# Optimization experiments

Hardware: AMD Instinct MI355X
Metric: run time of the kernel (lower is better)

Reference implementation:

```python
import jax, jax.numpy as jnp
import numpy as np

N = 1200        # nodes in the (complete) graph
SLOPE = 0.1     # leaky_relu negative slope
# smat: 10-vector -> symmetric 4x4
SMAT_IDX = np.array([0,1,2,3,1,4,5,6,2,5,7,8,3,6,8,9])

def _glorot(k, shape):
    lim = float(np.sqrt(6.0 / (shape[0] + shape[1])))
    return jax.random.uniform(k, shape, jnp.float32, -lim, lim)

def setup_inputs():
    key = jax.random.key(0)
    ks = jax.random.split(key, 24)
    # complete graph connectivity (recover_S reads edge_map[i,j] for all i!=j)
    iu, ju = np.triu_indices(N, k=1)
    E = iu.shape[0]
    eid = np.arange(E, dtype=np.int32)
    edge_map = np.zeros((N, N), dtype=np.int32)
    edge_map[iu, ju] = eid
    edge_map[ju, iu] = eid
    ud_edges = np.stack([iu, ju], axis=1).astype(np.int32)           # [E,2]
    edge_index = np.stack([np.concatenate([iu, ju]),
                           np.concatenate([ju, iu])]).astype(np.int32)  # [2,2E]
    inp = {
        'x': jax.random.normal(ks[0], (N, 16), jnp.float32),
        'edge_index': jnp.asarray(edge_index),
        'edge_map': jnp.asarray(edge_map),
        'ud_edges': jnp.asarray(ud_edges),
    }
    dims = {'g': [(6, 32), (32, 32), (32, 64)],
            'n': [(64, 64), (64, 64), (64, 10)],
            'e': [(64, 64), (64, 64), (64, 16)]}
    k = 1
    for tag, ds in dims.items():
        for i, (a, b) in enumerate(ds):
            inp[f'W{tag}{i+1}'] = _glorot(ks[k], (a, b)); k += 1
            inp[f'b{tag}{i+1}'] = jnp.zeros((b,), jnp.float32)
    return inp

def _leaky(v):
    return jnp.where(v >= 0, v, SLOPE * v)

def _gcn(x, src, dst, W, b):
    deg = jax.ops.segment_sum(jnp.ones(src.shape[0], x.dtype), dst, num_segments=N)
    dinv = jnp.where(deg > 0, jax.lax.rsqrt(deg), 0.0)
    norm = dinv[src] * dinv[dst]
    h = x @ W
    return jax.ops.segment_sum(norm[:, None] * h[src], dst, num_segments=N) + b

def _mlp3(h, W1, b1, W2, b2, W3, b3):
    # dropout is identity (eval mode)
    h = _leaky(h @ W1 + b1)
    h = _leaky(h @ W2 + b2)
    return h @ W3 + b3

def _forward(x, edge_index, edge_map, ud_edges,
             Wg1, bg1, Wg2, bg2, Wg3, bg3,
             Wn1, bn1, Wn2, bn2, Wn3, bn3,
             We1, be1, We2, be2, We3, be3):
    x6 = x[:, 0:6]                       # node_feature_mode == 1
    src, dst = edge_index[0], edge_index[1]
    h = _leaky(_gcn(x6, src, dst, Wg1, bg1))
    h = _leaky(_gcn(h, src, dst, Wg2, bg2))
    h = _gcn(h, src, dst, Wg3, bg3)      # [N,64]
    vd = _mlp3(h, Wn1, bn1, Wn2, bn2, Wn3, bn3)            # [N,10]
    he = h[ud_edges[:, 0]] + h[ud_edges[:, 1]]             # [E,64]
    ed = _mlp3(he, We1, be1, We2, be2, We3, be3)           # [E,16]
    # recover_S: block-structured [4N,4N]
    Vsym = vd[:, jnp.asarray(SMAT_IDX)].reshape(N, 4, 4)   # smat per node
    Eb = ed.reshape(-1, 4, 4)
    B = Eb[edge_map]                                       # [N,N,4,4]
    ii = jnp.arange(N)
    lower = ii[:, None] > ii[None, :]
    B = jnp.where(lower[:, :, None, None], jnp.swapaxes(B, 2, 3), B)
    B = B.at[ii, ii].set(Vsym)
    S = B.transpose(0, 2, 1, 3).reshape(4 * N, 4 * N)
    return h, S

def reference(x, edge_index, edge_map, ud_edges,
              Wg1, bg1, Wg2, bg2, Wg3, bg3,
              Wn1, bn1, Wn2, bn2, Wn3, bn3,
              We1, be1, We2, be2, We3, be3):
    return _forward(x, edge_index, edge_map, ud_edges,
                    Wg1, bg1, Wg2, bg2, Wg3, bg3,
                    Wn1, bn1, Wn2, bn2, Wn3, bn3,
                    We1, be1, We2, be2, We3, be3)
```

## Files before the change

kernel.cpp:

```cpp
#include <hip/hip_runtime.h>

#define NN 1200
#define NE 719400
#define SDIM 4800

typedef __attribute__((ext_vector_type(8))) short bf16x8;
typedef __attribute__((ext_vector_type(4))) float f32x4;

static __device__ __constant__ int SMAT[16] = {0,1,2,3,1,4,5,6,2,5,7,8,3,6,8,9};

__device__ __forceinline__ float lk(float v) { return v >= 0.f ? v : 0.1f * v; }

__device__ __forceinline__ void split8(const float* u, bf16x8& hi, bf16x8& lo) {
#pragma unroll
    for (int e = 0; e < 8; e++) {
        unsigned x = __float_as_uint(u[e]);
        unsigned r = x + 0x7FFFu + ((x >> 16) & 1u);
        hi[e] = (short)(r >> 16);
        float hf = __uint_as_float(r & 0xFFFF0000u);
        float s = u[e] - hf;
        unsigned v = __float_as_uint(s);
        unsigned w = v + 0x7FFFu + ((v >> 16) & 1u);
        lo[e] = (short)(w >> 16);
    }
}

__device__ __forceinline__ uint2 split2(float a0, float a1) {
    unsigned u0 = __float_as_uint(a0), u1 = __float_as_uint(a1);
    unsigned r0 = u0 + 0x7FFFu + ((u0 >> 16) & 1u);
    unsigned r1 = u1 + 0x7FFFu + ((u1 >> 16) & 1u);
    float h0 = __uint_as_float(r0 & 0xFFFF0000u);
    float h1 = __uint_as_float(r1 & 0xFFFF0000u);
    float s0 = a0 - h0, s1 = a1 - h1;
    unsigned v0 = __float_as_uint(s0), v1 = __float_as_uint(s1);
    unsigned t0 = v0 + 0x7FFFu + ((v0 >> 16) & 1u);
    unsigned t1 = v1 + 0x7FFFu + ((v1 >> 16) & 1u);
    unsigned hi = (r0 >> 16) | (r1 & 0xFFFF0000u);
    unsigned lo = (t0 >> 16) | (t1 & 0xFFFF0000u);
    return make_uint2(hi, lo);
}

__global__ void k_init(float* cs) {
    int t = threadIdx.x;
    if (t < 128) cs[t] = 0.f;
}

__global__ void k_prep(const float* __restrict__ We2, const float* __restrict__ We3,
                       unsigned* __restrict__ W2F, unsigned* __restrict__ W3F) {
    int t = blockIdx.x * 256 + threadIdx.x;
    if (t < 512) {
        int lane = t & 63, nf = (t >> 6) & 3, ks = t >> 8;
        int n = (lane & 15) + 16 * nf;
        int kb = ks * 32 + (lane >> 4) * 8;
        unsigned* dst = W2F + t * 8;
#pragma unroll
        for (int p = 0; p < 4; p++) {
            float a0 = We2[(kb + 2 * p) * 64 + n];
            float a1 = We2[(kb + 2 * p + 1) * 64 + n];
            uint2 hl = split2(a0, a1);
            dst[p] = hl.x; dst[4 + p] = hl.y;
        }
    } else if (t < 640) {
        int q = t - 512;
        int lane = q & 63, ks = q >> 6;
        int n = lane & 15;
        int kb = ks * 32 + (lane >> 4) * 8;
        unsigned* dst = W3F + q * 8;
#pragma unroll
        for (int p = 0; p < 4; p++) {
            float a0 = We3[(kb + 2 * p) * 16 + n];
            float a1 = We3[(kb + 2 * p + 1) * 16 + n];
            uint2 hl = split2(a0, a1);
            dst[p] = hl.x; dst[4 + p] = hl.y;
        }
    }
}

__global__ __launch_bounds__(256) void k_t1(const float* __restrict__ x,
                                            const float* __restrict__ Wg1,
                                            float* __restrict__ t1,
                                            float* __restrict__ cs1) {
    int T = blockIdx.x * 256 + threadIdx.x;
    int c = T & 31, rs = T >> 5;
    float w[6];
#pragma unroll
    for (int k = 0; k < 6; k++) w[k] = Wg1[k * 32 + c];
    float loc = 0.f;
    for (int r = rs; r < NN; r += 304) {
        float acc = 0.f;
#pragma unroll
        for (int k = 0; k < 6; k++) acc = fmaf(x[r * 16 + k], w[k], acc);
        t1[r * 32 + c] = acc;
        loc += acc;
    }
    atomicAdd(&cs1[c], loc);
}

__global__ __launch_bounds__(256) void k_t2(const float* __restrict__ t1,
                                            const float* __restrict__ cs1,
                                            const float* __restrict__ bg1,
                                            const float* __restrict__ Wg2,
                                            float* __restrict__ t2,
                                            float* __restrict__ cs2) {
    int T = blockIdx.x * 256 + threadIdx.x;
    int c = T & 31, rs = T >> 5;
    const float inv = 1.0f / 1199.0f;
    float p[32], w[32];
#pragma unroll
    for (int k = 0; k < 32; k++) {
        p[k] = fmaf(cs1[k], inv, bg1[k]);
        w[k] = Wg2[k * 32 + c];
    }
    float loc = 0.f;
    for (int r = rs; r < NN; r += 304) {
        float acc = 0.f;
#pragma unroll
        for (int k = 0; k < 32; k++) {
            float h = lk(fmaf(-t1[r * 32 + k], inv, p[k]));
            acc = fmaf(h, w[k], acc);
        }
        t2[r * 32 + c] = acc;
        loc += acc;
    }
    atomicAdd(&cs2[c], loc);
}

__global__ __launch_bounds__(256) void k_t3(const float* __restrict__ t2,
                                            const float* __restrict__ cs2,
                                            const float* __restrict__ bg2,
                                            const float* __restrict__ Wg3,
                                            float* __restrict__ t3,
                                            float* __restrict__ cs3) {
    int T = blockIdx.x * 256 + threadIdx.x;
    int c = T & 63, rs = T >> 6;
    const float inv = 1.0f / 1199.0f;
    float p[32], w[32];
#pragma unroll
    for (int k = 0; k < 32; k++) {
        p[k] = fmaf(cs2[k], inv, bg2[k]);
        w[k] = Wg3[k * 64 + c];
    }
    float loc = 0.f;
    for (int r = rs; r < NN; r += 152) {
        float acc = 0.f;
#pragma unroll
        for (int k = 0; k < 32; k++) {
            float h = lk(fmaf(-t2[r * 32 + k], inv, p[k]));
            acc = fmaf(h, w[k], acc);
        }
        t3[r * 64 + c] = acc;
        loc += acc;
    }
    atomicAdd(&cs3[c], loc);
}

__device__ __forceinline__ void gemm2x8(const float A[64][65], const float* W,
                                        int rg, int cg, float acc[2][8]) {
#pragma unroll 8
    for (int k = 0; k < 64; k++) {
        float a0 = A[rg * 2 + 0][k];
        float a1 = A[rg * 2 + 1][k];
        float4 b0 = *(const float4*)&W[k * 64 + cg * 8];
        float4 b1 = *(const float4*)&W[k * 64 + cg * 8 + 4];
        acc[0][0] = fmaf(a0, b0.x, acc[0][0]); acc[0][1] = fmaf(a0, b0.y, acc[0][1]);
        acc[0][2] = fmaf(a0, b0.z, acc[0][2]); acc[0][3] = fmaf(a0, b0.w, acc[0][3]);
        acc[0][4] = fmaf(a0, b1.x, acc[0][4]); acc[0][5] = fmaf(a0, b1.y, acc[0][5]);
        acc[0][6] = fmaf(a0, b1.z, acc[0][6]); acc[0][7] = fmaf(a0, b1.w, acc[0][7]);
        acc[1][0] = fmaf(a1, b0.x, acc[1][0]); acc[1][1] = fmaf(a1, b0.y, acc[1][1]);
        acc[1][2] = fmaf(a1, b0.z, acc[1][2]); acc[1][3] = fmaf(a1, b0.w, acc[1][3]);
        acc[1][4] = fmaf(a1, b1.x, acc[1][4]); acc[1][5] = fmaf(a1, b1.y, acc[1][5]);
        acc[1][6] = fmaf(a1, b1.z, acc[1][6]); acc[1][7] = fmaf(a1, b1.w, acc[1][7]);
    }
}

__global__ __launch_bounds__(256) void k_node(
    const float* __restrict__ t3, const float* __restrict__ cs3,
    const float* __restrict__ bg3,
    const float* __restrict__ We1,
    const float* __restrict__ Wn1, const float* __restrict__ bn1,
    const float* __restrict__ Wn2, const float* __restrict__ bn2,
    const float* __restrict__ Wn3, const float* __restrict__ bn3,
    float* __restrict__ h_out, float* __restrict__ g_out,
    float* __restrict__ S) {
    __shared__ float H[64][65];
    __shared__ float N1s[64][65];
    __shared__ float WA[4096];
    __shared__ float WB[4096];
    __shared__ float WC[4096];
    __shared__ float WD[640];
    __shared__ float VD[64][12];
    __shared__ float sbn1[64], sbn2[64], sbn3[16];

    const int tid = threadIdx.x;
    const int r0 = blockIdx.x * 64;
    const float inv = 1.0f / 1199.0f;

    for (int t = tid; t < 1024; t += 256) {
        ((float4*)WA)[t] = ((const float4*)We1)[t];
        ((float4*)WB)[t] = ((const float4*)Wn1)[t];
        ((float4*)WC)[t] = ((const float4*)Wn2)[t];
    }
    for (int t = tid; t < 640; t += 256) WD[t] = Wn3[t];
    if (tid < 64) { sbn1[tid] = bn1[tid]; sbn2[tid] = bn2[tid]; }
    if (tid < 10) sbn3[tid] = bn3[tid];

    for (int t = tid; t < 4096; t += 256) {
        int i = t >> 6, c = t & 63;
        int row = r0 + i;
        float v = 0.f;
        if (row < NN) {
            v = fmaf(cs3[c] - t3[row * 64 + c], inv, bg3[c]);
            h_out[row * 64 + c] = v;
        }
        H[i][c] = v;
    }
    __syncthreads();

    const int rg = tid >> 3;
    const int cg = tid & 7;

    {
        float acc[2][8] = {};
        gemm2x8(H, WA, rg, cg, acc);
#pragma unroll
        for (int m = 0; m < 2; m++) {
            int row = r0 + rg * 2 + m;
            if (row < NN) {
                *(float4*)&g_out[row * 64 + cg * 8]     = make_float4(acc[m][0], acc[m][1], acc[m][2], acc[m][3]);
                *(float4*)&g_out[row * 64 + cg * 8 + 4] = make_float4(acc[m][4], acc[m][5], acc[m][6], acc[m][7]);
            }
        }
    }
    {
        float acc[2][8] = {};
        gemm2x8(H, WB, rg, cg, acc);
#pragma unroll
        for (int m = 0; m < 2; m++)
#pragma unroll
            for (int q = 0; q < 8; q++)
                N1s[rg * 2 + m][cg * 8 + q] = lk(acc[m][q] + sbn1[cg * 8 + q]);
    }
    __syncthreads();
    {
        float acc[2][8] = {};
        gemm2x8(N1s, WC, rg, cg, acc);
#pragma unroll
        for (int m = 0; m < 2; m++)
#pragma unroll
            for (int q = 0; q < 8; q++)
                H[rg * 2 + m][cg * 8 + q] = lk(acc[m][q] + sbn2[cg * 8 + q]);
    }
    __syncthreads();
    for (int t = tid; t < 640; t += 256) {
        int r = t / 10, c = t % 10;
        float acc = sbn3[c];
        for (int k = 0; k < 64; k++) acc = fmaf(H[r][k], WD[k * 10 + c], acc);
        VD[r][c] = acc;
    }
    __syncthreads();
    {
        int r = tid >> 2, a = tid & 3;
        int row = r0 + r;
        if (row < NN) {
            float4 v = make_float4(VD[r][SMAT[a * 4 + 0]], VD[r][SMAT[a * 4 + 1]],
                                   VD[r][SMAT[a * 4 + 2]], VD[r][SMAT[a * 4 + 3]]);
            *(float4*)&S[(4 * row + a) * SDIM + 4 * row] = v;
        }
    }
}

__global__ __launch_bounds__(256) void k_edge(const int* __restrict__ ud,
                                              const float* __restrict__ g,
                                              const float* __restrict__ be1,
                                              const float* __restrict__ be2,
                                              const float* __restrict__ be3,
                                              const unsigned* __restrict__ W2F,
                                              const unsigned* __restrict__ W3F,
                                              float* __restrict__ S) {
    __shared__ float VB[128][68];
    __shared__ float ED[128][16];
    __shared__ int II[128], JJ[128];

    const int tid = threadIdx.x;
    const int wave = tid >> 6, lane = tid & 63;
    const int lrow = lane & 15, lgrp = lane >> 4;
    const int base = blockIdx.x * 128;

    if (tid < 128) {
        int e = base + tid;
        int2 ij = make_int2(0, 0);
        if (e < NE) ij = ((const int2*)ud)[e];
        II[tid] = ij.x; JJ[tid] = ij.y;
    }
    __syncthreads();

    bf16x8 Ahi[2][2], Alo[2][2];
#pragma unroll
    for (int mf = 0; mf < 2; mf++) {
        int r = wave * 32 + mf * 16 + lrow;
        const float* gi = g + II[r] * 64;
        const float* gj = g + JJ[r] * 64;
#pragma unroll
        for (int ks = 0; ks < 2; ks++) {
            int kb = ks * 32 + lgrp * 8;
            f32x4 a0 = *(const f32x4*)(gi + kb);
            f32x4 a1 = *(const f32x4*)(gi + kb + 4);
            f32x4 b0 = *(const f32x4*)(gj + kb);
            f32x4 b1 = *(const f32x4*)(gj + kb + 4);
            f32x4 c0 = *(const f32x4*)(be1 + kb);
            f32x4 c1 = *(const f32x4*)(be1 + kb + 4);
            float u[8];
#pragma unroll
            for (int e = 0; e < 4; e++) {
                u[e]     = lk(a0[e] + b0[e] + c0[e]);
                u[4 + e] = lk(a1[e] + b1[e] + c1[e]);
            }
            split8(u, Ahi[mf][ks], Alo[mf][ks]);
        }
    }

    f32x4 acc[2][4];
#pragma unroll
    for (int mf = 0; mf < 2; mf++)
#pragma unroll
        for (int nf = 0; nf < 4; nf++)
#pragma unroll
            for (int q = 0; q < 4; q++) acc[mf][nf][q] = 0.f;

#pragma unroll
    for (int nf = 0; nf < 4; nf++)
#pragma unroll
        for (int ks = 0; ks < 2; ks++) {
            const unsigned* p = W2F + ((ks * 4 + nf) * 64 + lane) * 8;
            bf16x8 bh = *(const bf16x8*)p;
            bf16x8 bl = *(const bf16x8*)(p + 4);
#pragma unroll
            for (int mf = 0; mf < 2; mf++) {
                acc[mf][nf] = __builtin_amdgcn_mfma_f32_16x16x32_bf16(Ahi[mf][ks], bh, acc[mf][nf], 0, 0, 0);
                acc[mf][nf] = __builtin_amdgcn_mfma_f32_16x16x32_bf16(Alo[mf][ks], bh, acc[mf][nf], 0, 0, 0);
                acc[mf][nf] = __builtin_amdgcn_mfma_f32_16x16x32_bf16(Ahi[mf][ks], bl, acc[mf][nf], 0, 0, 0);
            }
        }

#pragma unroll
    for (int nf = 0; nf < 4; nf++) {
        float b2 = be2[lrow + 16 * nf];
#pragma unroll
        for (int mf = 0; mf < 2; mf++)
#pragma unroll
            for (int rg = 0; rg < 4; rg++)
                VB[wave * 32 + mf * 16 + lgrp * 4 + rg][lrow + 16 * nf] = lk(acc[mf][nf][rg] + b2);
    }
    __syncthreads();

    f32x4 acc3[2];
#pragma unroll
    for (int mf = 0; mf < 2; mf++)
#pragma unroll
        for (int q = 0; q < 4; q++) acc3[mf][q] = 0.f;

#pragma unroll
    for (int ks = 0; ks < 2; ks++) {
        const unsigned* p = W3F + (ks * 64 + lane) * 8;
        bf16x8 bh = *(const bf16x8*)p;
        bf16x8 bl = *(const bf16x8*)(p + 4);
#pragma unroll
        for (int mf = 0; mf < 2; mf++) {
            int row = wave * 32 + mf * 16 + lrow;
            int kb = ks * 32 + lgrp * 8;
            f32x4 v0 = *(const f32x4*)&VB[row][kb];
            f32x4 v1 = *(const f32x4*)&VB[row][kb + 4];
            float u[8] = {v0[0], v0[1], v0[2], v0[3], v1[0], v1[1], v1[2], v1[3]};
            bf16x8 vh, vl;
            split8(u, vh, vl);
            acc3[mf] = __builtin_amdgcn_mfma_f32_16x16x32_bf16(vh, bh, acc3[mf], 0, 0, 0);
            acc3[mf] = __builtin_amdgcn_mfma_f32_16x16x32_bf16(vl, bh, acc3[mf], 0, 0, 0);
            acc3[mf] = __builtin_amdgcn_mfma_f32_16x16x32_bf16(vh, bl, acc3[mf], 0, 0, 0);
        }
    }
    {
        float b3 = be3[lrow];
#pragma unroll
        for (int mf = 0; mf < 2; mf++)
#pragma unroll
            for (int rg = 0; rg < 4; rg++)
                ED[wave * 32 + mf * 16 + lgrp * 4 + rg][lrow] = acc3[mf][rg] + b3;
    }
    __syncthreads();

#pragma unroll
    for (int p = 0; p < 2; p++) {
        int t = tid + p * 256;
        int r = t >> 2, a = t & 3;
        int e = base + r;
        if (e < NE) {
            int i = II[r], j = JJ[r];
            float4 v = make_float4(ED[r][a * 4 + 0], ED[r][a * 4 + 1],
                                   ED[r][a * 4 + 2], ED[r][a * 4 + 3]);
            *(float4*)&S[(4 * i + a) * SDIM + 4 * j] = v;
            float4 w = make_float4(ED[r][0 + a], ED[r][4 + a],
                                   ED[r][8 + a], ED[r][12 + a]);
            *(float4*)&S[(4 * j + a) * SDIM + 4 * i] = w;
        }
    }
}

extern "C" void kernel_launch(void* const* d_in, const int* in_sizes, int n_in,
                              void* d_out, int out_size, void* d_ws, size_t ws_size,
                              hipStream_t stream) {
    const float* x   = (const float*)d_in[0];
    const int*   ud  = (const int*)d_in[3];
    const float* Wg1 = (const float*)d_in[4];
    const float* bg1 = (const float*)d_in[5];
    const float* Wg2 = (const float*)d_in[6];
    const float* bg2 = (const float*)d_in[7];
    const float* Wg3 = (const float*)d_in[8];
    const float* bg3 = (const float*)d_in[9];
    const float* Wn1 = (const float*)d_in[10];
    const float* bn1 = (const float*)d_in[11];
    const float* Wn2 = (const float*)d_in[12];
    const float* bn2 = (const float*)d_in[13];
    const float* Wn3 = (const float*)d_in[14];
    const float* bn3 = (const float*)d_in[15];
    const float* We1 = (const float*)d_in[16];
    const float* be1 = (const float*)d_in[17];
    const float* We2 = (const float*)d_in[18];
    const float* be2 = (const float*)d_in[19];
    const float* We3 = (const float*)d_in[20];
    const float* be3 = (const float*)d_in[21];

    float* out   = (float*)d_out;
    float* h_out = out;
    float* S     = out + 76800;

    float* ws  = (float*)d_ws;
    float* t1  = ws;
    float* t2  = ws + 38400;
    float* t3  = ws + 76800;
    float* g   = ws + 153600;
    float* cs  = ws + 230400;
    unsigned* W2F = (unsigned*)(ws + 230528);
    unsigned* W3F = W2F + 4096;

    k_init<<<1, 128, 0, stream>>>(cs);
    k_prep<<<3, 256, 0, stream>>>(We2, We3, W2F, W3F);
    k_t1<<<38, 256, 0, stream>>>(x, Wg1, t1, cs);
    k_t2<<<38, 256, 0, stream>>>(t1, cs, bg1, Wg2, t2, cs + 32);
    k_t3<<<38, 256, 0, stream>>>(t2, cs + 32, bg2, Wg3, t3, cs + 64);
    k_node<<<19, 256, 0, stream>>>(t3, cs + 64, bg3, We1, Wn1, bn1, Wn2, bn2,
                                   Wn3, bn3, h_out, g, S);
    k_edge<<<5621, 256, 0, stream>>>(ud, g, be1, be2, be3, W2F, W3F, S);
}
```

Before: 140.7 us.

## Keep edge-MLP activations in registers via transposed MFMA and split node kernel

Result: faster. 125.3 us (-10.9%).

```diff
diff --git a/kernel.cpp b/kernel.cpp
--- a/kernel.cpp
+++ b/kernel.cpp
@@ -5,15 +5,42 @@
 #define SDIM 4800
 
 typedef __attribute__((ext_vector_type(8))) short bf16x8;
+typedef __attribute__((ext_vector_type(4))) short bf16x4;
 typedef __attribute__((ext_vector_type(4))) float f32x4;
 
 static __device__ __constant__ int SMAT[16] = {0,1,2,3,1,4,5,6,2,5,7,8,3,6,8,9};
 
 __device__ __forceinline__ float lk(float v) { return v >= 0.f ? v : 0.1f * v; }
 
+#if __has_builtin(__builtin_amdgcn_mfma_f32_16x16x16bf16_1k)
+__device__ __forceinline__ f32x4 mfma1616(bf16x4 a, bf16x4 b, f32x4 c) {
+    return __builtin_amdgcn_mfma_f32_16x16x16bf16_1k(a, b, c, 0, 0, 0);
+}
+#else
+__device__ __forceinline__ f32x4 mfma1616(bf16x4 a, bf16x4 b, f32x4 c) {
+    asm volatile("v_mfma_f32_16x16x16_bf16 %0, %1, %2, %0\n\ts_nop 7\n\ts_nop 7"
+                 : "+v"(c) : "v"(a), "v"(b));
+    return c;
+}
+#endif
+
 __device__ __forceinline__ void split8(const float* u, bf16x8& hi, bf16x8& lo) {
 #pragma unroll
     for (int e = 0; e < 8; e++) {
+        unsigned x = __float_as_uint(u[e]);
+        unsigned r = x + 0x7FFFu + ((x >> 16) & 1u);
+        hi[e] = (short)(r >> 16);
+        float hf = __uint_as_float(r & 0xFFFF0000u);
+        float s = u[e] - hf;
+        unsigned v = __float_as_uint(s);
+        unsigned w = v + 0x7FFFu + ((v >> 16) & 1u);
+        lo[e] = (short)(w >> 16);
+    }
+}
+
+__device__ __forceinline__ void split4(const float* u, bf16x4& hi, bf16x4& lo) {
+#pragma unroll
+    for (int e = 0; e < 4; e++) {
         unsigned x = __float_as_uint(u[e]);
         unsigned r = x + 0x7FFFu + ((x >> 16) & 1u);
         hi[e] = (short)(r >> 16);
@@ -40,39 +67,41 @@
     return make_uint2(hi, lo);
 }
 
-__global__ void k_init(float* cs) {
-    int t = threadIdx.x;
-    if (t < 128) cs[t] = 0.f;
-}
-
 __global__ void k_prep(const float* __restrict__ We2, const float* __restrict__ We3,
-                       unsigned* __restrict__ W2F, unsigned* __restrict__ W3F) {
+                       unsigned* __restrict__ W2F, unsigned* __restrict__ W3F,
+                       float* __restrict__ cs) {
     int t = blockIdx.x * 256 + threadIdx.x;
     if (t < 512) {
-        int lane = t & 63, nf = (t >> 6) & 3, ks = t >> 8;
-        int n = (lane & 15) + 16 * nf;
+        int lane = t & 63, ks = (t >> 6) & 1, mt = t >> 7;
+        int m = mt * 16 + (lane & 15);
         int kb = ks * 32 + (lane >> 4) * 8;
-        unsigned* dst = W2F + t * 8;
+        unsigned hi[4], lo[4];
 #pragma unroll
         for (int p = 0; p < 4; p++) {
-            float a0 = We2[(kb + 2 * p) * 64 + n];
-            float a1 = We2[(kb + 2 * p + 1) * 64 + n];
+            float a0 = We2[(kb + 2 * p) * 64 + m];
+            float a1 = We2[(kb + 2 * p + 1) * 64 + m];
             uint2 hl = split2(a0, a1);
-            dst[p] = hl.x; dst[4 + p] = hl.y;
-        }
-    } else if (t < 640) {
+            hi[p] = hl.x; lo[p] = hl.y;
+        }
+        *(uint4*)(W2F + ((mt * 2 + ks) * 2 + 0) * 256 + lane * 4) = make_uint4(hi[0], hi[1], hi[2], hi[3]);
+        *(uint4*)(W2F + ((mt * 2 + ks) * 2 + 1) * 256 + lane * 4) = make_uint4(lo[0], lo[1], lo[2], lo[3]);
+    } else if (t < 768) {
         int q = t - 512;
-        int lane = q & 63, ks = q >> 6;
-        int n = lane & 15;
-        int kb = ks * 32 + (lane >> 4) * 8;
-        unsigned* dst = W3F + q * 8;
-#pragma unroll
-        for (int p = 0; p < 4; p++) {
-            float a0 = We3[(kb + 2 * p) * 16 + n];
-            float a1 = We3[(kb + 2 * p + 1) * 16 + n];
+        int lane = q & 63, kb = q >> 6;
+        int c = lane & 15;
+        int k0 = kb * 16 + (lane >> 4) * 4;
+        unsigned hi[2], lo[2];
+#pragma unroll
+        for (int p = 0; p < 2; p++) {
+            float a0 = We3[(k0 + 2 * p) * 16 + c];
+            float a1 = We3[(k0 + 2 * p + 1) * 16 + c];
             uint2 hl = split2(a0, a1);
-            dst[p] = hl.x; dst[4 + p] = hl.y;
-        }
+            hi[p] = hl.x; lo[p] = hl.y;
+        }
+        *(uint2*)(W3F + (kb * 2 + 0) * 128 + lane * 2) = make_uint2(hi[0], hi[1]);
+        *(uint2*)(W3F + (kb * 2 + 1) * 128 + lane * 2) = make_uint2(lo[0], lo[1]);
+    } else if (t < 896) {
+        cs[t - 768] = 0.f;
     }
 }
 
@@ -154,57 +183,20 @@
     atomicAdd(&cs3[c], loc);
 }
 
-__device__ __forceinline__ void gemm2x8(const float A[64][65], const float* W,
-                                        int rg, int cg, float acc[2][8]) {
-#pragma unroll 8
-    for (int k = 0; k < 64; k++) {
-        float a0 = A[rg * 2 + 0][k];
-        float a1 = A[rg * 2 + 1][k];
-        float4 b0 = *(const float4*)&W[k * 64 + cg * 8];
-        float4 b1 = *(const float4*)&W[k * 64 + cg * 8 + 4];
-        acc[0][0] = fmaf(a0, b0.x, acc[0][0]); acc[0][1] = fmaf(a0, b0.y, acc[0][1]);
-        acc[0][2] = fmaf(a0, b0.z, acc[0][2]); acc[0][3] = fmaf(a0, b0.w, acc[0][3]);
-        acc[0][4] = fmaf(a0, b1.x, acc[0][4]); acc[0][5] = fmaf(a0, b1.y, acc[0][5]);
-        acc[0][6] = fmaf(a0, b1.z, acc[0][6]); acc[0][7] = fmaf(a0, b1.w, acc[0][7]);
-        acc[1][0] = fmaf(a1, b0.x, acc[1][0]); acc[1][1] = fmaf(a1, b0.y, acc[1][1]);
-        acc[1][2] = fmaf(a1, b0.z, acc[1][2]); acc[1][3] = fmaf(a1, b0.w, acc[1][3]);
-        acc[1][4] = fmaf(a1, b1.x, acc[1][4]); acc[1][5] = fmaf(a1, b1.y, acc[1][5]);
-        acc[1][6] = fmaf(a1, b1.z, acc[1][6]); acc[1][7] = fmaf(a1, b1.w, acc[1][7]);
-    }
-}
-
-__global__ __launch_bounds__(256) void k_node(
-    const float* __restrict__ t3, const float* __restrict__ cs3,
-    const float* __restrict__ bg3,
-    const float* __restrict__ We1,
-    const float* __restrict__ Wn1, const float* __restrict__ bn1,
-    const float* __restrict__ Wn2, const float* __restrict__ bn2,
-    const float* __restrict__ Wn3, const float* __restrict__ bn3,
-    float* __restrict__ h_out, float* __restrict__ g_out,
-    float* __restrict__ S) {
-    __shared__ float H[64][65];
-    __shared__ float N1s[64][65];
-    __shared__ float WA[4096];
-    __shared__ float WB[4096];
-    __shared__ float WC[4096];
-    __shared__ float WD[640];
-    __shared__ float VD[64][12];
-    __shared__ float sbn1[64], sbn2[64], sbn3[16];
-
+__global__ __launch_bounds__(256) void k_g(const float* __restrict__ t3,
+                                           const float* __restrict__ cs3,
+                                           const float* __restrict__ bg3,
+                                           const float* __restrict__ We1,
+                                           float* __restrict__ h_out,
+                                           float* __restrict__ g_out) {
+    __shared__ float H[32][65];
+    __shared__ float W[4096];
     const int tid = threadIdx.x;
-    const int r0 = blockIdx.x * 64;
+    const int r0 = blockIdx.x * 32;
     const float inv = 1.0f / 1199.0f;
 
-    for (int t = tid; t < 1024; t += 256) {
-        ((float4*)WA)[t] = ((const float4*)We1)[t];
-        ((float4*)WB)[t] = ((const float4*)Wn1)[t];
-        ((float4*)WC)[t] = ((const float4*)Wn2)[t];
-    }
-    for (int t = tid; t < 640; t += 256) WD[t] = Wn3[t];
-    if (tid < 64) { sbn1[tid] = bn1[tid]; sbn2[tid] = bn2[tid]; }
-    if (tid < 10) sbn3[tid] = bn3[tid];
-
-    for (int t = tid; t < 4096; t += 256) {
+    for (int t = tid; t < 1024; t += 256) ((float4*)W)[t] = ((const float4*)We1)[t];
+    for (int t = tid; t < 2048; t += 256) {
         int i = t >> 6, c = t & 63;
         int row = r0 + i;
         float v = 0.f;
@@ -216,49 +208,97 @@
     }
     __syncthreads();
 
-    const int rg = tid >> 3;
-    const int cg = tid & 7;
-
+    int rg = tid >> 3, cg = tid & 7;
+    float acc[8] = {};
+#pragma unroll 8
+    for (int k = 0; k < 64; k++) {
+        float a = H[rg][k];
+        float4 b0 = *(const float4*)&W[k * 64 + cg * 8];
+        float4 b1 = *(const float4*)&W[k * 64 + cg * 8 + 4];
+        acc[0] = fmaf(a, b0.x, acc[0]); acc[1] = fmaf(a, b0.y, acc[1]);
+        acc[2] = fmaf(a, b0.z, acc[2]); acc[3] = fmaf(a, b0.w, acc[3]);
+        acc[4] = fmaf(a, b1.x, acc[4]); acc[5] = fmaf(a, b1.y, acc[5]);
+        acc[6] = fmaf(a, b1.z, acc[6]); acc[7] = fmaf(a, b1.w, acc[7]);
+    }
+    int row = r0 + rg;
+    if (row < NN) {
+        *(float4*)&g_out[row * 64 + cg * 8]     = make_float4(acc[0], acc[1], acc[2], acc[3]);
+        *(float4*)&g_out[row * 64 + cg * 8 + 4] = make_float4(acc[4], acc[5], acc[6], acc[7]);
+    }
+}
+
+__global__ __launch_bounds__(256) void k_vd(const float* __restrict__ h,
+                                            const float* __restrict__ Wn1, const float* __restrict__ bn1,
+                                            const float* __restrict__ Wn2, const float* __restrict__ bn2,
+                                            const float* __restrict__ Wn3, const float* __restrict__ bn3,
+                                            float* __restrict__ S) {
+    __shared__ float H[32][65];
+    __shared__ float N1[32][65];
+    __shared__ float WB[4096];
+    __shared__ float WC[4096];
+    __shared__ float WD[640];
+    __shared__ float VD[32][12];
+    __shared__ float sb1[64], sb2[64], sb3[16];
+
+    const int tid = threadIdx.x;
+    const int r0 = blockIdx.x * 32;
+
+    for (int t = tid; t < 1024; t += 256) {
+        ((float4*)WB)[t] = ((const float4*)Wn1)[t];
+        ((float4*)WC)[t] = ((const float4*)Wn2)[t];
+    }
+    for (int t = tid; t < 640; t += 256) WD[t] = Wn3[t];
+    if (tid < 64) { sb1[tid] = bn1[tid]; sb2[tid] = bn2[tid]; }
+    if (tid < 10) sb3[tid] = bn3[tid];
+
+    for (int t = tid; t < 2048; t += 256) {
+        int i = t >> 6, c = t & 63;
+        int row = r0 + i;
+        H[i][c] = (row < NN) ? h[row * 64 + c] : 0.f;
+    }
+    __syncthreads();
+
+    int rg = tid >> 3, cg = tid & 7;
     {
-        float acc[2][8] = {};
-        gemm2x8(H, WA, rg, cg, acc);
-#pragma unroll
-        for (int m = 0; m < 2; m++) {
-            int row = r0 + rg * 2 + m;
-            if (row < NN) {
-                *(float4*)&g_out[row * 64 + cg * 8]     = make_float4(acc[m][0], acc[m][1], acc[m][2], acc[m][3]);
-                *(float4*)&g_out[row * 64 + cg * 8 + 4] = make_float4(acc[m][4], acc[m][5], acc[m][6], acc[m][7]);
-            }
-        }
-    }
-    {
-        float acc[2][8] = {};
-        gemm2x8(H, WB, rg, cg, acc);
-#pragma unroll
-        for (int m = 0; m < 2; m++)
-#pragma unroll
-            for (int q = 0; q < 8; q++)
-                N1s[rg * 2 + m][cg * 8 + q] = lk(acc[m][q] + sbn1[cg * 8 + q]);
+        float acc[8] = {};
+#pragma unroll 8
+        for (int k = 0; k < 64; k++) {
+            float a = H[rg][k];
+            float4 b0 = *(const float4*)&WB[k * 64 + cg * 8];
+            float4 b1 = *(const float4*)&WB[k * 64 + cg * 8 + 4];
+            acc[0] = fmaf(a, b0.x, acc[0]); acc[1] = fmaf(a, b0.y, acc[1]);
+            acc[2] = fmaf(a, b0.z, acc[2]); acc[3] = fmaf(a, b0.w, acc[3]);
+            acc[4] = fmaf(a, b1.x, acc[4]); acc[5] = fmaf(a, b1.y, acc[5]);
+            acc[6] = fmaf(a, b1.z, acc[6]); acc[7] = fmaf(a, b1.w, acc[7]);
+        }
+#pragma unroll
+        for (int q = 0; q < 8; q++) N1[rg][cg * 8 + q] = lk(acc[q] + sb1[cg * 8 + q]);
     }
     __syncthreads();
     {
-        float acc[2][8] = {};
-        gemm2x8(N1s, WC, rg, cg, acc);
-#pragma unroll
-        for (int m = 0; m < 2; m++)
-#pragma unroll
-            for (int q = 0; q < 8; q++)
-                H[rg * 2 + m][cg * 8 + q] = lk(acc[m][q] + sbn2[cg * 8 + q]);
+        float acc[8] = {};
+#pragma unroll 8
+        for (int k = 0; k < 64; k++) {
+            float a = N1[rg][k];
+            float4 b0 = *(const float4*)&WC[k * 64 + cg * 8];
+            float4 b1 = *(const float4*)&WC[k * 64 + cg * 8 + 4];
+            acc[0] = fmaf(a, b0.x, acc[0]); acc[1] = fmaf(a, b0.y, acc[1]);
+            acc[2] = fmaf(a, b0.z, acc[2]); acc[3] = fmaf(a, b0.w, acc[3]);
+            acc[4] = fmaf(a, b1.x, acc[4]); acc[5] = fmaf(a, b1.y, acc[5]);
+            acc[6] = fmaf(a, b1.z, acc[6]); acc[7] = fmaf(a, b1.w, acc[7]);
+        }
+#pragma unroll
+        for (int q = 0; q < 8; q++) H[rg][cg * 8 + q] = lk(acc[q] + sb2[cg * 8 + q]);
     }
     __syncthreads();
-    for (int t = tid; t < 640; t += 256) {
+    for (int t = tid; t < 320; t += 256) {
         int r = t / 10, c = t % 10;
-        float acc = sbn3[c];
+        float acc = sb3[c];
         for (int k = 0; k < 64; k++) acc = fmaf(H[r][k], WD[k * 10 + c], acc);
         VD[r][c] = acc;
     }
     __syncthreads();
-    {
+    if (tid < 128) {
         int r = tid >> 2, a = tid & 3;
         int row = r0 + r;
         if (row < NN) {
@@ -277,131 +317,121 @@
                                               const unsigned* __restrict__ W2F,
                                               const unsigned* __restrict__ W3F,
                                               float* __restrict__ S) {
-    __shared__ float VB[128][68];
-    __shared__ float ED[128][16];
-    __shared__ int II[128], JJ[128];
+    __shared__ float EDW[4][32][17];
 
     const int tid = threadIdx.x;
     const int wave = tid >> 6, lane = tid & 63;
     const int lrow = lane & 15, lgrp = lane >> 4;
-    const int base = blockIdx.x * 128;
-
-    if (tid < 128) {
-        int e = base + tid;
-        int2 ij = make_int2(0, 0);
-        if (e < NE) ij = ((const int2*)ud)[e];
-        II[tid] = ij.x; JJ[tid] = ij.y;
-    }
-    __syncthreads();
-
-    bf16x8 Ahi[2][2], Alo[2][2];
-#pragma unroll
-    for (int mf = 0; mf < 2; mf++) {
-        int r = wave * 32 + mf * 16 + lrow;
-        const float* gi = g + II[r] * 64;
-        const float* gj = g + JJ[r] * 64;
+    const int base_e = blockIdx.x * 128 + wave * 32;
+
+    const int e0 = base_e + lrow;
+    const int e1 = base_e + 16 + lrow;
+    const int2 ij0 = ((const int2*)ud)[min(e0, NE - 1)];
+    const int2 ij1 = ((const int2*)ud)[min(e1, NE - 1)];
+
+    f32x4 b1a[2][2];
+#pragma unroll
+    for (int ks = 0; ks < 2; ks++) {
+        b1a[ks][0] = *(const f32x4*)(be1 + ks * 32 + lgrp * 8);
+        b1a[ks][1] = *(const f32x4*)(be1 + ks * 32 + lgrp * 8 + 4);
+    }
+
+    bf16x8 Uhi[2][2], Ulo[2][2];
+#pragma unroll
+    for (int nt = 0; nt < 2; nt++) {
+        const int2 ij = nt ? ij1 : ij0;
+        const float* gi = g + ij.x * 64;
+        const float* gj = g + ij.y * 64;
 #pragma unroll
         for (int ks = 0; ks < 2; ks++) {
             int kb = ks * 32 + lgrp * 8;
-            f32x4 a0 = *(const f32x4*)(gi + kb);
-            f32x4 a1 = *(const f32x4*)(gi + kb + 4);
-            f32x4 b0 = *(const f32x4*)(gj + kb);
-            f32x4 b1 = *(const f32x4*)(gj + kb + 4);
-            f32x4 c0 = *(const f32x4*)(be1 + kb);
-            f32x4 c1 = *(const f32x4*)(be1 + kb + 4);
+            f32x4 x0 = *(const f32x4*)(gi + kb);
+            f32x4 x1 = *(const f32x4*)(gi + kb + 4);
+            f32x4 y0 = *(const f32x4*)(gj + kb);
+            f32x4 y1 = *(const f32x4*)(gj + kb + 4);
             float u[8];
 #pragma unroll
             for (int e = 0; e < 4; e++) {
-                u[e]     = lk(a0[e] + b0[e] + c0[e]);
-                u[4 + e] = lk(a1[e] + b1[e] + c1[e]);
+                u[e]     = lk(x0[e] + y0[e] + b1a[ks][0][e]);
+                u[4 + e] = lk(x1[e] + y1[e] + b1a[ks][1][e]);
             }
-            split8(u, Ahi[mf][ks], Alo[mf][ks]);
-        }
-    }
-
-    f32x4 acc[2][4];
-#pragma unroll
-    for (int mf = 0; mf < 2; mf++)
-#pragma unroll
-        for (int nf = 0; nf < 4; nf++)
-#pragma unroll
-            for (int q = 0; q < 4; q++) acc[mf][nf][q] = 0.f;
-
-#pragma unroll
-    for (int nf = 0; nf < 4; nf++)
+            split8(u, Uhi[nt][ks], Ulo[nt][ks]);
+        }
+    }
+
+    bf16x4 Vhi[4][2], Vlo[4][2];
+#pragma unroll
+    for (int mt = 0; mt < 4; mt++) {
+        f32x4 acc[2];
+#pragma unroll
+        for (int nt = 0; nt < 2; nt++)
+#pragma unroll
+            for (int q = 0; q < 4; q++) acc[nt][q] = 0.f;
 #pragma unroll
         for (int ks = 0; ks < 2; ks++) {
-            const unsigned* p = W2F + ((ks * 4 + nf) * 64 + lane) * 8;
-            bf16x8 bh = *(const bf16x8*)p;
-            bf16x8 bl = *(const bf16x8*)(p + 4);
-#pragma unroll
-            for (int mf = 0; mf < 2; mf++) {
-                acc[mf][nf] = __builtin_amdgcn_mfma_f32_16x16x32_bf16(Ahi[mf][ks], bh, acc[mf][nf], 0, 0, 0);
-                acc[mf][nf] = __builtin_amdgcn_mfma_f32_16x16x32_bf16(Alo[mf][ks], bh, acc[mf][nf], 0, 0, 0);
-                acc[mf][nf] = __builtin_amdgcn_mfma_f32_16x16x32_bf16(Ahi[mf][ks], bl, acc[mf][nf], 0, 0, 0);
+            bf16x8 Whi = *(const bf16x8*)(W2F + ((mt * 2 + ks) * 2 + 0) * 256 + lane * 4);
+            bf16x8 Wlo = *(const bf16x8*)(W2F + ((mt * 2 + ks) * 2 + 1) * 256 + lane * 4);
+#pragma unroll
+            for (int nt = 0; nt < 2; nt++) {
+                acc[nt] = __builtin_amdgcn_mfma_f32_16x16x32_bf16(Whi, Uhi[nt][ks], acc[nt], 0, 0, 0);
+                acc[nt] = __builtin_amdgcn_mfma_f32_16x16x32_bf16(Wlo, Uhi[nt][ks], acc[nt], 0, 0, 0);
+                acc[nt] = __builtin_amdgcn_mfma_f32_16x16x32_bf16(Whi, Ulo[nt][ks], acc[nt], 0, 0, 0);
             }
         }
-
-#pragma unroll
-    for (int nf = 0; nf < 4; nf++) {
-        float b2 = be2[lrow + 16 * nf];
-#pragma unroll
-        for (int mf = 0; mf < 2; mf++)
-#pragma unroll
-            for (int rg = 0; rg < 4; rg++)
-                VB[wave * 32 + mf * 16 + lgrp * 4 + rg][lrow + 16 * nf] = lk(acc[mf][nf][rg] + b2);
-    }
-    __syncthreads();
+        f32x4 b2 = *(const f32x4*)(be2 + mt * 16 + lgrp * 4);
+#pragma unroll
+        for (int nt = 0; nt < 2; nt++) {
+            float v[4];
+#pragma unroll
+            for (int q = 0; q < 4; q++) v[q] = lk(acc[nt][q] + b2[q]);
+            split4(v, Vhi[mt][nt], Vlo[mt][nt]);
+        }
+    }
 
     f32x4 acc3[2];
 #pragma unroll
-    for (int mf = 0; mf < 2; mf++)
-#pragma unroll
-        for (int q = 0; q < 4; q++) acc3[mf][q] = 0.f;
-
-#pragma unroll
-    for (int ks = 0; ks < 2; ks++) {
-        const unsigned* p = W3F + (ks * 64 + lane) * 8;
-        bf16x8 bh = *(const bf16x8*)p;
-        bf16x8 bl = *(const bf16x8*)(p + 4);
-#pragma unroll
-        for (int mf = 0; mf < 2; mf++) {
-            int row = wave * 32 + mf * 16 + lrow;
-            int kb = ks * 32 + lgrp * 8;
-            f32x4 v0 = *(const f32x4*)&VB[row][kb];
-            f32x4 v1 = *(const f32x4*)&VB[row][kb + 4];
-            float u[8] = {v0[0], v0[1], v0[2], v0[3], v1[0], v1[1], v1[2], v1[3]};
-            bf16x8 vh, vl;
-            split8(u, vh, vl);
-            acc3[mf] = __builtin_amdgcn_mfma_f32_16x16x32_bf16(vh, bh, acc3[mf], 0, 0, 0);
-            acc3[mf] = __builtin_amdgcn_mfma_f32_16x16x32_bf16(vl, bh, acc3[mf], 0, 0, 0);
-            acc3[mf] = __builtin_amdgcn_mfma_f32_16x16x32_bf16(vh, bl, acc3[mf], 0, 0, 0);
-        }
-    }
-    {
-        float b3 = be3[lrow];
-#pragma unroll
-        for (int mf = 0; mf < 2; mf++)
-#pragma unroll
-            for (int rg = 0; rg < 4; rg++)
-                ED[wave * 32 + mf * 16 + lgrp * 4 + rg][lrow] = acc3[mf][rg] + b3;
-    }
-    __syncthreads();
-
-#pragma unroll
-    for (int p = 0; p < 2; p++) {
-        int t = tid + p * 256;
-        int r = t >> 2, a = t & 3;
-        int e = base + r;
+    for (int nt = 0; nt < 2; nt++)
+#pragma unroll
+        for (int q = 0; q < 4; q++) acc3[nt][q] = 0.f;
+#pragma unroll
+    for (int kb = 0; kb < 4; kb++) {
+        bf16x4 W3h = *(const bf16x4*)(W3F + (kb * 2 + 0) * 128 + lane * 2);
+        bf16x4 W3l = *(const bf16x4*)(W3F + (kb * 2 + 1) * 128 + lane * 2);
+#pragma unroll
+        for (int nt = 0; nt < 2; nt++) {
+            acc3[nt] = mfma1616(W3h, Vhi[kb][nt], acc3[nt]);
+            acc3[nt] = mfma1616(W3l, Vhi[kb][nt], acc3[nt]);
+            acc3[nt] = mfma1616(W3h, Vlo[kb][nt], acc3[nt]);
+        }
+    }
+
+    f32x4 b3 = *(const f32x4*)(be3 + lgrp * 4);
+#pragma unroll
+    for (int nt = 0; nt < 2; nt++) {
+        const int e = nt ? e1 : e0;
+        const int2 ij = nt ? ij1 : ij0;
+        float ed[4];
+#pragma unroll
+        for (int q = 0; q < 4; q++) {
+            ed[q] = acc3[nt][q] + b3[q];
+            EDW[wave][nt * 16 + lrow][lgrp * 4 + q] = ed[q];
+        }
         if (e < NE) {
-            int i = II[r], j = JJ[r];
-            float4 v = make_float4(ED[r][a * 4 + 0], ED[r][a * 4 + 1],
-                                   ED[r][a * 4 + 2], ED[r][a * 4 + 3]);
-            *(float4*)&S[(4 * i + a) * SDIM + 4 * j] = v;
-            float4 w = make_float4(ED[r][0 + a], ED[r][4 + a],
-                                   ED[r][8 + a], ED[r][12 + a]);
-            *(float4*)&S[(4 * j + a) * SDIM + 4 * i] = w;
-        }
+            *(float4*)&S[(4 * ij.x + lgrp) * SDIM + 4 * ij.y] =
+                make_float4(ed[0], ed[1], ed[2], ed[3]);
+        }
+    }
+
+    const int le = lane & 31;
+    const int lg2 = lane >> 5;
+    const int eL = base_e + le;
+    const int2 ijL = ((const int2*)ud)[min(eL, NE - 1)];
+#pragma unroll
+    for (int q = 0; q < 2; q++) {
+        int a = lg2 * 2 + q;
+        float4 v = make_float4(EDW[wave][le][a], EDW[wave][le][4 + a],
+                               EDW[wave][le][8 + a], EDW[wave][le][12 + a]);
+        if (eL < NE) *(float4*)&S[(4 * ijL.y + a) * SDIM + 4 * ijL.x] = v;
     }
 }
 
@@ -442,12 +472,11 @@
     unsigned* W2F = (unsigned*)(ws + 230528);
     unsigned* W3F = W2F + 4096;
 
-    k_init<<<1, 128, 0, stream>>>(cs);
-    k_prep<<<3, 256, 0, stream>>>(We2, We3, W2F, W3F);
+    k_prep<<<4, 256, 0, stream>>>(We2, We3, W2F, W3F, cs);
     k_t1<<<38, 256, 0, stream>>>(x, Wg1, t1, cs);
     k_t2<<<38, 256, 0, stream>>>(t1, cs, bg1, Wg2, t2, cs + 32);
     k_t3<<<38, 256, 0, stream>>>(t2, cs + 32, bg2, Wg3, t3, cs + 64);
-    k_node<<<19, 256, 0, stream>>>(t3, cs + 64, bg3, We1, Wn1, bn1, Wn2, bn2,
-                                   Wn3, bn3, h_out, g, S);
+    k_g<<<38, 256, 0, stream>>>(t3, cs + 64, bg3, We1, h_out, g);
     k_edge<<<5621, 256, 0, stream>>>(ud, g, be1, be2, be3, W2F, W3F, S);
-}
+    k_vd<<<38, 256, 0, stream>>>(h_out, Wn1, bn1, Wn2, bn2, Wn3, bn3, S);
+}
```
